# Performance work log

Measured on AMD Instinct MI355X. Metric: run time of the kernel, lower is better.

Reference implementation:

```python
import jax, jax.numpy as jnp
import numpy as np
import math

D = 2048            # fc_feat_size (hardcoded sqrt(2048) scale in source)
IMAGES = 20         # images_per_person
NEIGHBOR = 5        # neighbor_size (sliding window width)
T = IMAGES - NEIGHBOR + 1   # number of windows = 16
SCALE = 1.0 / math.sqrt(2048.0)


def _attention(x, Wq, bq, Wk, bk, Wv, bv):
    # x: [N, L, D] -> [N, L, D]; bmm-softmax-bmm as in source
    q = x @ Wq.T + bq
    k = x @ Wk.T + bk
    v = x @ Wv.T + bv
    dot = jnp.einsum('nld,nmd->nlm', q, k) * SCALE
    w = jax.nn.softmax(dot, axis=-1)
    return jnp.einsum('nlm,nmd->nld', w, v)


def _lstm_final(x, Wih, Whh, bih, bhh):
    # PyTorch-convention LSTM (gates i,f,g,o); x: [N, L, D] -> final hidden [N, H]
    N = x.shape[0]
    H = Whh.shape[1]
    xg = x @ Wih.T + (bih + bhh)   # [N, L, 4H] precompute input projections

    def step(carry, xt):
        h, c = carry
        gates = xt + h @ Whh.T
        i, f, g, o = jnp.split(gates, 4, axis=-1)
        c = jax.nn.sigmoid(f) * c + jax.nn.sigmoid(i) * jnp.tanh(g)
        h = jax.nn.sigmoid(o) * jnp.tanh(c)
        return (h, c), None

    init = (jnp.zeros((N, H), x.dtype), jnp.zeros((N, H), x.dtype))
    (h, _), _ = jax.lax.scan(step, init, jnp.swapaxes(xg, 0, 1))
    return h


def _layernorm(x, g, b, eps=1e-5):
    mu = jnp.mean(x, axis=-1, keepdims=True)
    var = jnp.var(x, axis=-1, keepdims=True)
    return (x - mu) * jax.lax.rsqrt(var + eps) * g + b


def setup_inputs() -> dict:
    key = jax.random.key(0)
    ks = iter(jax.random.split(key, 32))
    s = 0.02
    p = {}
    p['fc_feats'] = jax.random.normal(next(ks), (64, IMAGES, D), jnp.float32)
    for pre in ('nsa', 'sa'):
        for nm in ('Wq', 'Wk', 'Wv'):
            p[f'{pre}_{nm}'] = jax.random.normal(next(ks), (D, D), jnp.float32) * s
        for nm in ('bq', 'bk', 'bv'):
            p[f'{pre}_{nm}'] = jnp.zeros((D,), jnp.float32)
        p[f'{pre}_Wih'] = jax.random.normal(next(ks), (4 * D, D), jnp.float32) * s
        p[f'{pre}_Whh'] = jax.random.normal(next(ks), (4 * D, D), jnp.float32) * s
        p[f'{pre}_bih'] = jnp.zeros((4 * D,), jnp.float32)
        p[f'{pre}_bhh'] = jnp.zeros((4 * D,), jnp.float32)
    p['ln_g'] = jnp.ones((D,), jnp.float32)
    p['ln_b'] = jnp.zeros((D,), jnp.float32)
    return p


def reference(fc_feats,
              nsa_Wq, nsa_Wk, nsa_Wv, nsa_bq, nsa_bk, nsa_bv,
              nsa_Wih, nsa_Whh, nsa_bih, nsa_bhh,
              sa_Wq, sa_Wk, sa_Wv, sa_bq, sa_bk, sa_bv,
              sa_Wih, sa_Whh, sa_bih, sa_bhh,
              ln_g, ln_b):
    B = fc_feats.shape[0]
    # Sliding windows: window t covers images [t, t+NEIGHBOR) -> [B, T, W, D]
    idx = jnp.arange(T)[:, None] + jnp.arange(NEIGHBOR)[None, :]
    windows = fc_feats[:, idx]                       # [B, T, W, D]
    wflat = windows.reshape(B * T, NEIGHBOR, D)
    # NeighboringSelfAttention: attention within window + LSTM final state
    att = _attention(wflat, nsa_Wq, nsa_bq, nsa_Wk, nsa_bk, nsa_Wv, nsa_bv)
    nsa = _lstm_final(att, nsa_Wih, nsa_Whh, nsa_bih, nsa_bhh)  # [B*T, D]
    nsa_feats = nsa.reshape(B, T, D)
    new_nsa_feats = _layernorm(nsa_feats, ln_g, ln_b)
    # SelfAttention over the T window summaries + LSTM final state
    att2 = _attention(new_nsa_feats, sa_Wq, sa_bq, sa_Wk, sa_bk, sa_Wv, sa_bv)
    sa_feats = _lstm_final(att2, sa_Wih, sa_Whh, sa_bih, sa_bhh)  # [B, D]
    return (sa_feats, new_nsa_feats)
```

## Files before the change

kernel.cpp:

```cpp
#include <hip/hip_runtime.h>
#include <hip/hip_bf16.h>

typedef unsigned int  u32;
typedef unsigned short u16;

typedef __bf16 bf16x8 __attribute__((ext_vector_type(8)));
typedef float  f32x4  __attribute__((ext_vector_type(4)));

#define D2048 2048
#define SCALE 0.022097086912079612f

__device__ __forceinline__ u32 f2bfbits(float f) {
    u32 u = __float_as_uint(f);
    return (u + 0x7FFFu + ((u >> 16) & 1u)) >> 16;
}
__device__ __forceinline__ u32 pack2(float a, float b) {
    return f2bfbits(a) | (f2bfbits(b) << 16);
}
__device__ __forceinline__ float bf2f(u32 h) {
    return __uint_as_float(h << 16);
}
__device__ __forceinline__ void unpack8(uint4 v, float* f) {
    f[0] = bf2f(v.x & 0xFFFFu); f[1] = bf2f(v.x >> 16);
    f[2] = bf2f(v.y & 0xFFFFu); f[3] = bf2f(v.y >> 16);
    f[4] = bf2f(v.z & 0xFFFFu); f[5] = bf2f(v.z >> 16);
    f[6] = bf2f(v.w & 0xFFFFu); f[7] = bf2f(v.w >> 16);
}
__device__ __forceinline__ float sigmf(float x) { return 1.f / (1.f + __expf(-x)); }
__device__ __forceinline__ float tanhf_(float x) {
    x = fminf(15.f, fmaxf(-15.f, x));
    float e = __expf(2.f * x);
    return (e - 1.f) / (e + 1.f);
}

__device__ __forceinline__ void gload_lds16(const u16* g, u16* l) {
    __builtin_amdgcn_global_load_lds(
        (const __attribute__((address_space(1))) unsigned int*)g,
        (__attribute__((address_space(3))) unsigned int*)l,
        16, 0, 0);
}

struct CvtArgs {
    const float* src[8];
    u16*         dst[8];
    int          n4[8];
    int          nseg;
};
__global__ __launch_bounds__(256) void cvt_multi(CvtArgs a) {
    int stride = gridDim.x * 256;
    for (int s = 0; s < a.nseg; ++s) {
        const float4* S = reinterpret_cast<const float4*>(a.src[s]);
        uint2*        D = reinterpret_cast<uint2*>(a.dst[s]);
        int n4 = a.n4[s];
        for (int i = blockIdx.x * 256 + threadIdx.x; i < n4; i += stride) {
            float4 v = S[i];
            uint2 p;
            p.x = pack2(v.x, v.y);
            p.y = pack2(v.z, v.w);
            D[i] = p;
        }
    }
}

template <bool OUT_BF16>
__global__ __launch_bounds__(512, 2) void gemm256(const u16* __restrict__ A, int lda,
                                                  const u16* __restrict__ B,
                                                  void* __restrict__ C0,
                                                  int M, int N, int K) {
    __shared__ u16 Ab[2][16384];
    __shared__ u16 Bb[2][16384];

    const int tid  = threadIdx.x;
    const int lane = tid & 63;
    const int wid  = tid >> 6;
    const int wm   = wid >> 2;
    const int wn   = wid & 3;
    const int l15  = lane & 15, l4 = lane >> 4;
    const int rowBase = blockIdx.y * 256;
    const int colBase = blockIdx.x * 256;

    const int srow8 = lane >> 3;
    const int scw   = ((lane & 7) ^ srow8) * 8;
    const u16* gA = A + (size_t)(rowBase + wid * 8 + srow8) * lda + scw;
    const u16* gB = B + (size_t)(colBase + wid * 8 + srow8) * (size_t)K + scw;
    const int ldsW = wid * 512;

#define STAGE_A(buf, koff, q) \
    gload_lds16(gA + (size_t)((q) * 64) * lda + (koff), &Ab[buf][(q) * 4096 + ldsW])
#define STAGE_B(buf, koff, q) \
    gload_lds16(gB + (size_t)((q) * 64) * (size_t)K + (koff), &Bb[buf][(q) * 4096 + ldsW])

    f32x4 acc[8][4];
#pragma unroll
    for (int m = 0; m < 8; m++)
#pragma unroll
        for (int n = 0; n < 4; n++) acc[m][n] = f32x4{0.f, 0.f, 0.f, 0.f};

    const int nt = K >> 6;

#pragma unroll
    for (int q = 0; q < 4; ++q) { STAGE_A(0, 0, q); STAGE_B(0, 0, q); }

    const int swzA = (l15 & 7);

    for (int t = 0; t < nt; ++t) {
        const int cur = t & 1;
        const int nxt = cur ^ 1;
        const int kN  = (t + 1) << 6;
        const bool more = (t + 1 < nt);

        if (more) {
            STAGE_A(nxt, kN, 0);
            STAGE_A(nxt, kN, 1);
            asm volatile("s_waitcnt vmcnt(2)" ::: "memory");
        } else {
            asm volatile("s_waitcnt vmcnt(0)" ::: "memory");
        }
        __builtin_amdgcn_s_barrier();

        bf16x8 bfrag[4][2];
#pragma unroll
        for (int n = 0; n < 4; ++n)
#pragma unroll
            for (int kk = 0; kk < 2; ++kk)
                bfrag[n][kk] = *reinterpret_cast<const bf16x8*>(
                    &Bb[cur][(wn * 64 + n * 16 + l15) * 64 +
                             (((kk * 4 + l4) ^ swzA) * 8)]);

#pragma unroll
        for (int p = 0; p < 4; ++p) {
            bf16x8 afr[2][2];
#pragma unroll
            for (int mi = 0; mi < 2; ++mi)
#pragma unroll
                for (int kk = 0; kk < 2; ++kk)
                    afr[mi][kk] = *reinterpret_cast<const bf16x8*>(
                        &Ab[cur][(wm * 128 + (p * 2 + mi) * 16 + l15) * 64 +
                                 (((kk * 4 + l4) ^ swzA) * 8)]);
            if (more) {
                if (p == 0)      { STAGE_A(nxt, kN, 2); STAGE_A(nxt, kN, 3); }
                else if (p == 1) { STAGE_B(nxt, kN, 0); STAGE_B(nxt, kN, 1); }
                else if (p == 2) { STAGE_B(nxt, kN, 2); STAGE_B(nxt, kN, 3); }
            }
            __builtin_amdgcn_s_barrier();
            __builtin_amdgcn_sched_barrier(0);
            __builtin_amdgcn_s_setprio(1);
#pragma unroll
            for (int kk = 0; kk < 2; ++kk)
#pragma unroll
                for (int mi = 0; mi < 2; ++mi)
#pragma unroll
                    for (int n = 0; n < 4; ++n)
                        acc[p * 2 + mi][n] = __builtin_amdgcn_mfma_f32_16x16x32_bf16(
                            afr[mi][kk], bfrag[n][kk], acc[p * 2 + mi][n], 0, 0, 0);
            __builtin_amdgcn_s_setprio(0);
            __builtin_amdgcn_sched_barrier(0);
            __builtin_amdgcn_s_barrier();
        }
    }
#undef STAGE_A
#undef STAGE_B

#pragma unroll
    for (int m = 0; m < 8; ++m) {
        int row0 = rowBase + wm * 128 + m * 16 + l4 * 4;
#pragma unroll
        for (int n = 0; n < 4; ++n) {
            int col = colBase + wn * 64 + n * 16 + l15;
#pragma unroll
            for (int rr = 0; rr < 4; ++rr) {
                if (OUT_BF16)
                    ((u16*)C0)[(size_t)(row0 + rr) * N + col] = (u16)f2bfbits(acc[m][n][rr]);
                else
                    ((float*)C0)[(size_t)(row0 + rr) * N + col] = acc[m][n][rr];
            }
        }
    }
}

__global__ __launch_bounds__(256) void gemm_qkv(const u16* __restrict__ A,
                                                const u16* __restrict__ B0,
                                                const u16* __restrict__ B1,
                                                const u16* __restrict__ B2,
                                                const float* __restrict__ bias0,
                                                const float* __restrict__ bias1,
                                                const float* __restrict__ bias2,
                                                u16* __restrict__ Cout,
                                                size_t zCstride,
                                                int M, int N, int K) {
    __shared__ u16 Abuf[2][128 * 64];
    __shared__ u16 Bbuf[2][128 * 64];

    const int tid  = threadIdx.x;
    const int lane = tid & 63;
    const int wave = tid >> 6;
    const int wr   = (wave >> 1) * 64;
    const int wc   = (wave & 1) * 64;
    const int rowBase = blockIdx.y * 128;
    const int colBase = blockIdx.x * 128;
    const int l15 = lane & 15, l4 = lane >> 4;
    const int srow = lane >> 3;
    const int scol = (lane & 7) * 8;

    const int z = blockIdx.z;
    const u16* B      = (z == 0) ? B0 : ((z == 1) ? B1 : B2);
    const float* bias = (z == 0) ? bias0 : ((z == 1) ? bias1 : bias2);
    u16* C = Cout + (size_t)z * zCstride;

    const u16* ga = A + (size_t)(rowBase + wave * 32 + srow) * K + scol;
    const u16* gb = B + (size_t)(colBase + wave * 32 + srow) * K + scol;
    const int ldsOff = (wave * 32) * 64;

    f32x4 acc[4][4];
#pragma unroll
    for (int i = 0; i < 4; i++)
#pragma unroll
        for (int j = 0; j < 4; j++) acc[i][j] = f32x4{0.f, 0.f, 0.f, 0.f};

    const int nt = K >> 6;

#pragma unroll
    for (int i = 0; i < 4; ++i) {
        gload_lds16(ga + (size_t)(i * 8) * K, &Abuf[0][ldsOff + i * 8 * 64]);
        gload_lds16(gb + (size_t)(i * 8) * K, &Bbuf[0][ldsOff + i * 8 * 64]);
    }

    for (int t = 0; t < nt; ++t) {
        const int cur = t & 1;
        if (t + 1 < nt) {
            const int k1 = (t + 1) << 6;
#pragma unroll
            for (int i = 0; i < 4; ++i) {
                gload_lds16(ga + (size_t)(i * 8) * K + k1,
                            &Abuf[cur ^ 1][ldsOff + i * 8 * 64]);
                gload_lds16(gb + (size_t)(i * 8) * K + k1,
                            &Bbuf[cur ^ 1][ldsOff + i * 8 * 64]);
            }
            asm volatile("s_waitcnt vmcnt(8)" ::: "memory");
        } else {
            asm volatile("s_waitcnt vmcnt(0)" ::: "memory");
        }
        __builtin_amdgcn_s_barrier();
        __builtin_amdgcn_sched_barrier(0);
#pragma unroll
        for (int kk = 0; kk < 2; ++kk) {
            bf16x8 af[4], bfr[4];
#pragma unroll
            for (int i = 0; i < 4; i++) {
                af[i]  = *reinterpret_cast<const bf16x8*>(
                    &Abuf[cur][(wr + i * 16 + l15) * 64 + kk * 32 + l4 * 8]);
                bfr[i] = *reinterpret_cast<const bf16x8*>(
                    &Bbuf[cur][(wc + i * 16 + l15) * 64 + kk * 32 + l4 * 8]);
            }
#pragma unroll
            for (int i = 0; i < 4; i++)
#pragma unroll
                for (int j = 0; j < 4; j++)
                    acc[i][j] = __builtin_amdgcn_mfma_f32_16x16x32_bf16(af[i], bfr[j],
                                                                        acc[i][j], 0, 0, 0);
        }
        __builtin_amdgcn_sched_barrier(0);
        __builtin_amdgcn_s_barrier();
    }

#pragma unroll
    for (int i = 0; i < 4; i++) {
        int row0 = rowBase + wr + i * 16 + l4 * 4;
#pragma unroll
        for (int j = 0; j < 4; j++) {
            int col = colBase + wc + j * 16 + l15;
            float bv = bias[col];
#pragma unroll
            for (int rr = 0; rr < 4; rr++)
                C[(size_t)(row0 + rr) * N + col] = (u16)f2bfbits(acc[i][j][rr] + bv);
        }
    }
}

template <bool LAST>
__global__ __launch_bounds__(256) void gemm_gate128(
    const u16* __restrict__ A,
    const u16* __restrict__ B,
    const u16* __restrict__ xg,
    int xg_stride,
    const float* __restrict__ bih,
    const float* __restrict__ bhh,
    float* __restrict__ c,
    u16* __restrict__ hbf_out,
    float* __restrict__ hf,
    int K) {
    __shared__ u16 smem[32768];
    u16* Ab = smem;
    u16* Bb = smem + 16384;

    const int tid = threadIdx.x, lane = tid & 63, wave = tid >> 6;
    const int wr = (wave >> 1) * 64, wc = (wave & 1) * 64;
    const int l15 = lane & 15, l4 = lane >> 4;
    const int srow = lane >> 3, scol = (lane & 7) * 8;
    const int jBase = blockIdx.x * 32;
    const int rowBase = blockIdx.y * 128;

    const u16* ga = A + (size_t)(rowBase + wave * 32 + srow) * K + scol;
    const u16* gb[4];
#pragma unroll
    for (int i = 0; i < 4; ++i) {
        int lc = wave * 32 + i * 8 + srow;
        int br = jBase + (lc & 31) + (lc >> 5) * 2048;
        gb[i] = B + (size_t)br * K + scol;
    }
    const int ldsOff = (wave * 32) * 64;

    f32x4 acc[4][4];
#pragma unroll
    for (int i = 0; i < 4; i++)
#pragma unroll
        for (int j = 0; j < 4; j++) acc[i][j] = f32x4{0.f, 0.f, 0.f, 0.f};

    const int nt = K >> 6;
#pragma unroll
    for (int i = 0; i < 4; ++i) {
        gload_lds16(ga + (size_t)(i * 8) * K, &Ab[ldsOff + i * 8 * 64]);
        gload_lds16(gb[i], &Bb[ldsOff + i * 8 * 64]);
    }

    for (int t = 0; t < nt; ++t) {
        const int cur = (t & 1) * 8192;
        if (t + 1 < nt) {
            const int k1 = (t + 1) << 6;
            const int nxt = ((t + 1) & 1) * 8192;
#pragma unroll
            for (int i = 0; i < 4; ++i) {
                gload_lds16(ga + (size_t)(i * 8) * K + k1, &Ab[nxt + ldsOff + i * 8 * 64]);
                gload_lds16(gb[i] + k1, &Bb[nxt + ldsOff + i * 8 * 64]);
            }
            asm volatile("s_waitcnt vmcnt(8)" ::: "memory");
        } else {
            asm volatile("s_waitcnt vmcnt(0)" ::: "memory");
        }
        __builtin_amdgcn_s_barrier();
        __builtin_amdgcn_sched_barrier(0);
#pragma unroll
        for (int kk = 0; kk < 2; ++kk) {
            bf16x8 af[4], bfr[4];
#pragma unroll
            for (int i = 0; i < 4; i++) {
                af[i]  = *reinterpret_cast<const bf16x8*>(
                    &Ab[cur + (wr + i * 16 + l15) * 64 + kk * 32 + l4 * 8]);
                bfr[i] = *reinterpret_cast<const bf16x8*>(
                    &Bb[cur + (wc + i * 16 + l15) * 64 + kk * 32 + l4 * 8]);
            }
#pragma unroll
            for (int i = 0; i < 4; i++)
#pragma unroll
                for (int j = 0; j < 4; j++)
                    acc[i][j] = __builtin_amdgcn_mfma_f32_16x16x32_bf16(af[i], bfr[j],
                                                                        acc[i][j], 0, 0, 0);
        }
        __builtin_amdgcn_sched_barrier(0);
        __builtin_amdgcn_s_barrier();
    }

    float* Cs = (float*)smem;
#pragma unroll
    for (int i = 0; i < 4; i++)
#pragma unroll
        for (int j = 0; j < 4; j++)
#pragma unroll
            for (int rr = 0; rr < 4; rr++)
                Cs[(wr + i * 16 + l4 * 4 + rr) * 128 + (wc + j * 16 + l15)] =
                    acc[i][j][rr];
    __syncthreads();

    const int j  = tid & 31;
    const int rb = tid >> 5;
    const int gj = jBase + j;
    const float bi_ = bih[gj]        + bhh[gj];
    const float bf_ = bih[gj + 2048] + bhh[gj + 2048];
    const float bg_ = bih[gj + 4096] + bhh[gj + 4096];
    const float bo_ = bih[gj + 6144] + bhh[gj + 6144];
#pragma unroll
    for (int k = 0; k < 16; ++k) {
        int r = rb * 16 + k;
        int n = rowBase + r;
        const u16* xr = xg + (size_t)n * xg_stride;
        float gi = Cs[r * 128 + j]      + bf2f((u32)xr[gj])        + bi_;
        float gf = Cs[r * 128 + 32 + j] + bf2f((u32)xr[gj + 2048]) + bf_;
        float gg = Cs[r * 128 + 64 + j] + bf2f((u32)xr[gj + 4096]) + bg_;
        float go = Cs[r * 128 + 96 + j] + bf2f((u32)xr[gj + 6144]) + bo_;
        size_t idx = (size_t)n * 2048 + gj;
        float cc = c[idx];
        float cn = sigmf(gf) * cc + sigmf(gi) * tanhf_(gg);
        float hn = sigmf(go) * tanhf_(cn);
        c[idx] = cn;
        hbf_out[idx] = (u16)f2bfbits(hn);
        if (LAST) hf[idx] = hn;
    }
}

__global__ __launch_bounds__(256) void gemm_gate64(
    const u16* __restrict__ A,
    const u16* __restrict__ B,
    const u16* __restrict__ xg,
    int xg_stride,
    const float* __restrict__ bih,
    const float* __restrict__ bhh,
    float* __restrict__ c,
    u16* __restrict__ hbf_out,
    float* __restrict__ hf,
    int K) {
    __shared__ u16 smem[24576];
    u16* Ab = smem;
    u16* Bb = smem + 8192;

    const int tid = threadIdx.x, lane = tid & 63, wave = tid >> 6;
    const int l15 = lane & 15, l4 = lane >> 4;
    const int srow = lane >> 3, scol = (lane & 7) * 8;
    const int jBase = blockIdx.x * 32;

    const u16* ga = A + (size_t)(wave * 16 + srow) * K + scol;
    const u16* gb[4];
#pragma unroll
    for (int i = 0; i < 4; ++i) {
        int lc = wave * 32 + i * 8 + srow;
        int br = jBase + (lc & 31) + (lc >> 5) * 2048;
        gb[i] = B + (size_t)br * K + scol;
    }
    const int laOff = (wave * 16) * 64;
    const int lbOff = (wave * 32) * 64;

    f32x4 acc[4][2];
#pragma unroll
    for (int i = 0; i < 4; i++)
#pragma unroll
        for (int j = 0; j < 2; j++) acc[i][j] = f32x4{0.f, 0.f, 0.f, 0.f};

    const int nt = K >> 6;
#pragma unroll
    for (int i = 0; i < 2; ++i)
        gload_lds16(ga + (size_t)(i * 8) * K, &Ab[laOff + i * 8 * 64]);
#pragma unroll
    for (int i = 0; i < 4; ++i)
        gload_lds16(gb[i], &Bb[lbOff + i * 8 * 64]);

    for (int t = 0; t < nt; ++t) {
        const int curA = (t & 1) * 4096;
        const int curB = (t & 1) * 8192;
        if (t + 1 < nt) {
            const int k1 = (t + 1) << 6;
            const int nxA = ((t + 1) & 1) * 4096;
            const int nxB = ((t + 1) & 1) * 8192;
#pragma unroll
            for (int i = 0; i < 2; ++i)
                gload_lds16(ga + (size_t)(i * 8) * K + k1, &Ab[nxA + laOff + i * 8 * 64]);
#pragma unroll
            for (int i = 0; i < 4; ++i)
                gload_lds16(gb[i] + k1, &Bb[nxB + lbOff + i * 8 * 64]);
            asm volatile("s_waitcnt vmcnt(6)" ::: "memory");
        } else {
            asm volatile("s_waitcnt vmcnt(0)" ::: "memory");
        }
        __builtin_amdgcn_s_barrier();
        __builtin_amdgcn_sched_barrier(0);
#pragma unroll
        for (int kk = 0; kk < 2; ++kk) {
            bf16x8 af[4], bfr[2];
#pragma unroll
            for (int i = 0; i < 4; i++)
                af[i] = *reinterpret_cast<const bf16x8*>(
                    &Ab[curA + (i * 16 + l15) * 64 + kk * 32 + l4 * 8]);
#pragma unroll
            for (int j = 0; j < 2; j++)
                bfr[j] = *reinterpret_cast<const bf16x8*>(
                    &Bb[curB + (wave * 32 + j * 16 + l15) * 64 + kk * 32 + l4 * 8]);
#pragma unroll
            for (int i = 0; i < 4; i++)
#pragma unroll
                for (int j = 0; j < 2; j++)
                    acc[i][j] = __builtin_amdgcn_mfma_f32_16x16x32_bf16(af[i], bfr[j],
                                                                        acc[i][j], 0, 0, 0);
        }
        __builtin_amdgcn_sched_barrier(0);
        __builtin_amdgcn_s_barrier();
    }

    float* Cs = (float*)smem;
#pragma unroll
    for (int i = 0; i < 4; i++)
#pragma unroll
        for (int j = 0; j < 2; j++)
#pragma unroll
            for (int rr = 0; rr < 4; rr++)
                Cs[(i * 16 + l4 * 4 + rr) * 128 + (wave * 32 + j * 16 + l15)] =
                    acc[i][j][rr];
    __syncthreads();

    const int j  = tid & 31;
    const int rb = tid >> 5;
    const int gj = jBase + j;
    const float bi_ = bih[gj]        + bhh[gj];
    const float bf_ = bih[gj + 2048] + bhh[gj + 2048];
    const float bg_ = bih[gj + 4096] + bhh[gj + 4096];
    const float bo_ = bih[gj + 6144] + bhh[gj + 6144];
#pragma unroll
    for (int k = 0; k < 8; ++k) {
        int n = rb * 8 + k;
        const u16* xr = xg + (size_t)n * xg_stride;
        float gi = Cs[n * 128 + j]      + bf2f((u32)xr[gj])        + bi_;
        float gf = Cs[n * 128 + 32 + j] + bf2f((u32)xr[gj + 2048]) + bf_;
        float gg = Cs[n * 128 + 64 + j] + bf2f((u32)xr[gj + 4096]) + bg_;
        float go = Cs[n * 128 + 96 + j] + bf2f((u32)xr[gj + 6144]) + bo_;
        size_t idx = (size_t)n * 2048 + gj;
        float cc = c[idx];
        float cn = sigmf(gf) * cc + sigmf(gi) * tanhf_(gg);
        float hn = sigmf(go) * tanhf_(cn);
        c[idx] = cn;
        hbf_out[idx] = (u16)f2bfbits(hn);
        if (hf) hf[idx] = hn;
    }
}

__global__ __launch_bounds__(256) void lstm_gate0(const u16* __restrict__ xg,
                                                  int xg_stride,
                                                  const float* __restrict__ bih,
                                                  const float* __restrict__ bhh,
                                                  float* __restrict__ c,
                                                  u16* __restrict__ hbf,
                                                  int rows) {
    int idx = blockIdx.x * 256 + threadIdx.x;
    int total = rows * 512;
    if (idx >= total) return;
    int n  = idx >> 9;
    int j4 = (idx & 511) * 4;

    const u16* xr = xg + (size_t)n * xg_stride + j4;
    float4 gi, gf, gg, go;
    {
        uint2 ri = *reinterpret_cast<const uint2*>(xr);
        uint2 rg = *reinterpret_cast<const uint2*>(xr + 4096);
        uint2 ro = *reinterpret_cast<const uint2*>(xr + 6144);
        gi = {bf2f(ri.x & 0xFFFFu), bf2f(ri.x >> 16), bf2f(ri.y & 0xFFFFu), bf2f(ri.y >> 16)};
        gg = {bf2f(rg.x & 0xFFFFu), bf2f(rg.x >> 16), bf2f(rg.y & 0xFFFFu), bf2f(rg.y >> 16)};
        go = {bf2f(ro.x & 0xFFFFu), bf2f(ro.x >> 16), bf2f(ro.y & 0xFFFFu), bf2f(ro.y >> 16)};
    }
    float4 bi1 = *reinterpret_cast<const float4*>(bih + j4);
    float4 bg1 = *reinterpret_cast<const float4*>(bih + 4096 + j4);
    float4 bo1 = *reinterpret_cast<const float4*>(bih + 6144 + j4);
    float4 bi2 = *reinterpret_cast<const float4*>(bhh + j4);
    float4 bg2 = *reinterpret_cast<const float4*>(bhh + 4096 + j4);
    float4 bo2 = *reinterpret_cast<const float4*>(bhh + 6144 + j4);

    gi.x += bi1.x + bi2.x; gi.y += bi1.y + bi2.y; gi.z += bi1.z + bi2.z; gi.w += bi1.w + bi2.w;
    gg.x += bg1.x + bg2.x; gg.y += bg1.y + bg2.y; gg.z += bg1.z + bg2.z; gg.w += bg1.w + bg2.w;
    go.x += bo1.x + bo2.x; go.y += bo1.y + bo2.y; go.z += bo1.z + bo2.z; go.w += bo1.w + bo2.w;

    float cx = sigmf(gi.x) * tanhf_(gg.x);
    float cy = sigmf(gi.y) * tanhf_(gg.y);
    float cz = sigmf(gi.z) * tanhf_(gg.z);
    float cw = sigmf(gi.w) * tanhf_(gg.w);
    float hx = sigmf(go.x) * tanhf_(cx);
    float hy = sigmf(go.y) * tanhf_(cy);
    float hz = sigmf(go.z) * tanhf_(cz);
    float hw_ = sigmf(go.w) * tanhf_(cw);

    float4 co = {cx, cy, cz, cw};
    *reinterpret_cast<float4*>(c + (size_t)n * 2048 + j4) = co;
    uint2 hp;
    hp.x = pack2(hx, hy);
    hp.y = pack2(hz, hw_);
    *reinterpret_cast<uint2*>(hbf + (size_t)n * 2048 + j4) = hp;
}

__global__ __launch_bounds__(256) void attn_win5(const u16* __restrict__ q0,
                                                 const u16* __restrict__ k0,
                                                 const u16* __restrict__ v0,
                                                 u16* __restrict__ att) {
    int n = blockIdx.x;
    int b = n >> 4, t = n & 15;
    int tid = threadIdx.x, lane = tid & 63, wave = tid >> 6;
    int d0 = tid * 8;
    size_t base = (size_t)(b * 20 + t) * D2048;

    float qv[5][8];
#pragma unroll
    for (int i = 0; i < 5; i++) {
        uint4 v = *reinterpret_cast<const uint4*>(q0 + base + (size_t)i * D2048 + d0);
        unpack8(v, qv[i]);
    }
    float part[25];
#pragma unroll
    for (int p = 0; p < 25; p++) part[p] = 0.f;
#pragma unroll
    for (int m = 0; m < 5; m++) {
        float kv[8];
        uint4 v = *reinterpret_cast<const uint4*>(k0 + base + (size_t)m * D2048 + d0);
        unpack8(v, kv);
#pragma unroll
        for (int l = 0; l < 5; l++)
#pragma unroll
            for (int j = 0; j < 8; j++) part[l * 5 + m] += qv[l][j] * kv[j];
    }
#pragma unroll
    for (int p = 0; p < 25; p++) {
        float s = part[p];
#pragma unroll
        for (int msk = 32; msk; msk >>= 1) s += __shfl_xor(s, msk, 64);
        part[p] = s;
    }
    __shared__ float wred[4][25];
    __shared__ float wmat[25];
    if (lane == 0) {
#pragma unroll
        for (int p = 0; p < 25; p++) wred[wave][p] = part[p];
    }
    __syncthreads();
    if (tid < 5) {
        int l = tid;
        float dv[5], mx = -1e30f;
#pragma unroll
        for (int m = 0; m < 5; m++) {
            dv[m] = (wred[0][l * 5 + m] + wred[1][l * 5 + m] + wred[2][l * 5 + m] +
                     wred[3][l * 5 + m]) * SCALE;
            mx = fmaxf(mx, dv[m]);
        }
        float ssum = 0.f;
#pragma unroll
        for (int m = 0; m < 5; m++) { dv[m] = __expf(dv[m] - mx); ssum += dv[m]; }
        float inv = 1.f / ssum;
#pragma unroll
        for (int m = 0; m < 5; m++) wmat[l * 5 + m] = dv[m] * inv;
    }
    __syncthreads();

    float oacc[5][8];
#pragma unroll
    for (int l = 0; l < 5; l++)
#pragma unroll
        for (int j = 0; j < 8; j++) oacc[l][j] = 0.f;
#pragma unroll
    for (int m = 0; m < 5; m++) {
        float vv[8];
        uint4 v = *reinterpret_cast<const uint4*>(v0 + base + (size_t)m * D2048 + d0);
        unpack8(v, vv);
#pragma unroll
        for (int l = 0; l < 5; l++) {
            float w = wmat[l * 5 + m];
#pragma unroll
            for (int j = 0; j < 8; j++) oacc[l][j] += w * vv[j];
        }
    }
#pragma unroll
    for (int l = 0; l < 5; l++) {
        uint4 p;
        p.x = pack2(oacc[l][0], oacc[l][1]);
        p.y = pack2(oacc[l][2], oacc[l][3]);
        p.z = pack2(oacc[l][4], oacc[l][5]);
        p.w = pack2(oacc[l][6], oacc[l][7]);
        *reinterpret_cast<uint4*>(att + (size_t)(n * 5 + l) * D2048 + d0) = p;
    }
}

__global__ __launch_bounds__(256) void attn_seq16(const u16* __restrict__ q2,
                                                  const u16* __restrict__ k2,
                                                  const u16* __restrict__ v2,
                                                  u16* __restrict__ att2) {
    int r = blockIdx.x;
    int b = r >> 4;
    int tid = threadIdx.x, lane = tid & 63, wave = tid >> 6;
    int d0 = tid * 8;
    size_t kbase = (size_t)b * 16 * D2048;

    float qv[8];
    {
        uint4 v = *reinterpret_cast<const uint4*>(q2 + (size_t)r * D2048 + d0);
        unpack8(v, qv);
    }
    float part[16];
#pragma unroll
    for (int m = 0; m < 16; m++) part[m] = 0.f;
#pragma unroll
    for (int m = 0; m < 16; m++) {
        float kv[8];
        uint4 v = *reinterpret_cast<const uint4*>(k2 + kbase + (size_t)m * D2048 + d0);
        unpack8(v, kv);
#pragma unroll
        for (int j = 0; j < 8; j++) part[m] += qv[j] * kv[j];
    }
#pragma unroll
    for (int m = 0; m < 16; m++) {
        float s = part[m];
#pragma unroll
        for (int msk = 32; msk; msk >>= 1) s += __shfl_xor(s, msk, 64);
        part[m] = s;
    }
    __shared__ float wred[4][16];
    __shared__ float wmat[16];
    if (lane == 0) {
#pragma unroll
        for (int m = 0; m < 16; m++) wred[wave][m] = part[m];
    }
    __syncthreads();
    if (tid == 0) {
        float dv[16], mx = -1e30f;
#pragma unroll
        for (int m = 0; m < 16; m++) {
            dv[m] = (wred[0][m] + wred[1][m] + wred[2][m] + wred[3][m]) * SCALE;
            mx = fmaxf(mx, dv[m]);
        }
        float ssum = 0.f;
#pragma unroll
        for (int m = 0; m < 16; m++) { dv[m] = __expf(dv[m] - mx); ssum += dv[m]; }
        float inv = 1.f / ssum;
#pragma unroll
        for (int m = 0; m < 16; m++) wmat[m] = dv[m] * inv;
    }
    __syncthreads();

    float oacc[8];
#pragma unroll
    for (int j = 0; j < 8; j++) oacc[j] = 0.f;
#pragma unroll
    for (int m = 0; m < 16; m++) {
        float vv[8];
        uint4 v = *reinterpret_cast<const uint4*>(v2 + kbase + (size_t)m * D2048 + d0);
        unpack8(v, vv);
        float w = wmat[m];
#pragma unroll
        for (int j = 0; j < 8; j++) oacc[j] += w * vv[j];
    }
    uint4 p;
    p.x = pack2(oacc[0], oacc[1]);
    p.y = pack2(oacc[2], oacc[3]);
    p.z = pack2(oacc[4], oacc[5]);
    p.w = pack2(oacc[6], oacc[7]);
    *reinterpret_cast<uint4*>(att2 + (size_t)r * D2048 + d0) = p;
}

__global__ __launch_bounds__(256) void layernorm_k(const float* __restrict__ x,
                                                   const float* __restrict__ g,
                                                   const float* __restrict__ b,
                                                   float* __restrict__ y,
                                                   u16* __restrict__ ybf) {
    int row = blockIdx.x;
    int tid = threadIdx.x, lane = tid & 63, wave = tid >> 6;
    const float* xr = x + (size_t)row * D2048;
    int j = tid * 8;
    float4 v1 = *reinterpret_cast<const float4*>(xr + j);
    float4 v2 = *reinterpret_cast<const float4*>(xr + j + 4);
    float s  = v1.x + v1.y + v1.z + v1.w + v2.x + v2.y + v2.z + v2.w;
    float s2 = v1.x * v1.x + v1.y * v1.y + v1.z * v1.z + v1.w * v1.w +
               v2.x * v2.x + v2.y * v2.y + v2.z * v2.z + v2.w * v2.w;
#pragma unroll
    for (int msk = 32; msk; msk >>= 1) {
        s  += __shfl_xor(s, msk, 64);
        s2 += __shfl_xor(s2, msk, 64);
    }
    __shared__ float red[4][2];
    if (lane == 0) { red[wave][0] = s; red[wave][1] = s2; }
    __syncthreads();
    s  = red[0][0] + red[1][0] + red[2][0] + red[3][0];
    s2 = red[0][1] + red[1][1] + red[2][1] + red[3][1];
    float mu  = s * (1.f / 2048.f);
    float var = s2 * (1.f / 2048.f) - mu * mu;
    float rs  = __frsqrt_rn(var + 1e-5f);

    float4 g1 = *reinterpret_cast<const float4*>(g + j);
    float4 g2 = *reinterpret_cast<const float4*>(g + j + 4);
    float4 b1 = *reinterpret_cast<const float4*>(b + j);
    float4 b2 = *reinterpret_cast<const float4*>(b + j + 4);
    float o[8];
    o[0] = (v1.x - mu) * rs * g1.x + b1.x;
    o[1] = (v1.y - mu) * rs * g1.y + b1.y;
    o[2] = (v1.z - mu) * rs * g1.z + b1.z;
    o[3] = (v1.w - mu) * rs * g1.w + b1.w;
    o[4] = (v2.x - mu) * rs * g2.x + b2.x;
    o[5] = (v2.y - mu) * rs * g2.y + b2.y;
    o[6] = (v2.z - mu) * rs * g2.z + b2.z;
    o[7] = (v2.w - mu) * rs * g2.w + b2.w;
    float4 o1 = {o[0], o[1], o[2], o[3]};
    float4 o2 = {o[4], o[5], o[6], o[7]};
    float* yr = y + (size_t)row * D2048;
    *reinterpret_cast<float4*>(yr + j)     = o1;
    *reinterpret_cast<float4*>(yr + j + 4) = o2;
    uint4 p;
    p.x = pack2(o[0], o[1]);
    p.y = pack2(o[2], o[3]);
    p.z = pack2(o[4], o[5]);
    p.w = pack2(o[6], o[7]);
    *reinterpret_cast<uint4*>(ybf + (size_t)row * D2048 + j) = p;
}

static inline void launch_qkv(hipStream_t s, const u16* A, const u16* Wq,
                              const u16* Wk, const u16* Wv, const float* bq,
                              const float* bk, const float* bv, u16* out,
                              int M, int N, int K) {
    dim3 grid(N / 128, M / 128, 3);
    gemm_qkv<<<grid, 256, 0, s>>>(A, Wq, Wk, Wv, bq, bk, bv, out,
                                  (size_t)M * N, M, N, K);
}

extern "C" void kernel_launch(void* const* d_in, const int* in_sizes, int n_in,
                              void* d_out, int out_size, void* d_ws, size_t ws_size,
                              hipStream_t stream) {
    const float* fc      = (const float*)d_in[0];
    const float* nsa_Wq  = (const float*)d_in[1];
    const float* nsa_Wk  = (const float*)d_in[2];
    const float* nsa_Wv  = (const float*)d_in[3];
    const float* nsa_bq  = (const float*)d_in[4];
    const float* nsa_bk  = (const float*)d_in[5];
    const float* nsa_bv  = (const float*)d_in[6];
    const float* nsa_Wih = (const float*)d_in[7];
    const float* nsa_Whh = (const float*)d_in[8];
    const float* nsa_bih = (const float*)d_in[9];
    const float* nsa_bhh = (const float*)d_in[10];
    const float* sa_Wq   = (const float*)d_in[11];
    const float* sa_Wk   = (const float*)d_in[12];
    const float* sa_Wv   = (const float*)d_in[13];
    const float* sa_bq   = (const float*)d_in[14];
    const float* sa_bk   = (const float*)d_in[15];
    const float* sa_bv   = (const float*)d_in[16];
    const float* sa_Wih  = (const float*)d_in[17];
    const float* sa_Whh  = (const float*)d_in[18];
    const float* sa_bih  = (const float*)d_in[19];
    const float* sa_bhh  = (const float*)d_in[20];
    const float* ln_g    = (const float*)d_in[21];
    const float* ln_b    = (const float*)d_in[22];

    float* outF   = (float*)d_out;
    float* out_sa = outF;
    float* out_ln = outF + 131072;

    char* W = (char*)d_ws;
    u16* W_q   = (u16*)(W + 0);
    u16* W_k   = (u16*)(W + 8388608);
    u16* W_v   = (u16*)(W + 16777216);
    u16* W_ih  = (u16*)(W + 25165824);
    u16* W_hh1 = (u16*)(W + 58720256);
    u16* W_hh2 = (u16*)(W + 92274688);
    u16*   Xbf  = (u16*)(W + 125829120);
    u16*   q0   = (u16*)(W + 131072000);
    u16*   att1 = (u16*)(W + 146800640);
    u16*   xg   = (u16*)(W + 167772160);
    float* h1    = (float*)(W + 0);
    float* c1    = (float*)(W + 8388608);
    u16*   hbfA  = (u16*)(W + 16777216);
    u16*   hbfB  = (u16*)(W + 131072000);
    u16*   lnbf  = Xbf;
    u16*   q2    = q0;
    u16*   att2  = att1;
    float* c2    = (float*)(W + 148373504);
    u16*   h2bfA = (u16*)(W + 148897792);
    u16*   h2bfB = (u16*)(W + 149422080);

    {
        CvtArgs a{};
        a.src[0] = fc;      a.dst[0] = Xbf;   a.n4[0] = 655360;
        a.src[1] = nsa_Wq;  a.dst[1] = W_q;   a.n4[1] = 1048576;
        a.src[2] = nsa_Wk;  a.dst[2] = W_k;   a.n4[2] = 1048576;
        a.src[3] = nsa_Wv;  a.dst[3] = W_v;   a.n4[3] = 1048576;
        a.src[4] = nsa_Wih; a.dst[4] = W_ih;  a.n4[4] = 4194304;
        a.src[5] = nsa_Whh; a.dst[5] = W_hh1; a.n4[5] = 4194304;
        a.src[6] = sa_Whh;  a.dst[6] = W_hh2; a.n4[6] = 4194304;
        a.nseg = 7;
        cvt_multi<<<2048, 256, 0, stream>>>(a);
    }

    launch_qkv(stream, Xbf, W_q, W_k, W_v, nsa_bq, nsa_bk, nsa_bv, q0, 1280, 2048, 2048);

    attn_win5<<<1024, 256, 0, stream>>>(q0, q0 + 2621440, q0 + 5242880, att1);

    gemm256<true><<<dim3(32, 20), 512, 0, stream>>>(att1, 2048, W_ih, xg,
                                                    5120, 8192, 2048);

    lstm_gate0<<<2048, 256, 0, stream>>>(xg, 40960, nsa_bih, nsa_bhh, c1, hbfA, 1024);
    {
        u16* hin = hbfA;
        for (int t = 1; t < 5; ++t) {
            u16* hout = (t & 1) ? hbfB : hbfA;
            if (t == 4)
                gemm_gate128<true><<<dim3(64, 8), 256, 0, stream>>>(
                    hin, W_hh1, xg + (size_t)t * 8192, 40960, nsa_bih, nsa_bhh,
                    c1, hout, h1, 2048);
            else
                gemm_gate128<false><<<dim3(64, 8), 256, 0, stream>>>(
                    hin, W_hh1, xg + (size_t)t * 8192, 40960, nsa_bih, nsa_bhh,
                    c1, hout, nullptr, 2048);
            hin = hout;
        }
    }

    layernorm_k<<<1024, 256, 0, stream>>>(h1, ln_g, ln_b, out_ln, lnbf);

    {
        CvtArgs a{};
        a.src[0] = sa_Wq;  a.dst[0] = W_q;  a.n4[0] = 1048576;
        a.src[1] = sa_Wk;  a.dst[1] = W_k;  a.n4[1] = 1048576;
        a.src[2] = sa_Wv;  a.dst[2] = W_v;  a.n4[2] = 1048576;
        a.src[3] = sa_Wih; a.dst[3] = W_ih; a.n4[3] = 4194304;
        a.nseg = 4;
        cvt_multi<<<2048, 256, 0, stream>>>(a);
    }

    launch_qkv(stream, lnbf, W_q, W_k, W_v, sa_bq, sa_bk, sa_bv, q2, 1024, 2048, 2048);

    attn_seq16<<<1024, 256, 0, stream>>>(q2, q2 + 2097152, q2 + 4194304, att2);

    gemm256<true><<<dim3(32, 4), 512, 0, stream>>>(att2, 2048, W_ih, xg,
                                                   1024, 8192, 2048);

    lstm_gate0<<<128, 256, 0, stream>>>(xg, 131072, sa_bih, sa_bhh, c2, h2bfA, 64);
    {
        u16* hin = h2bfA;
        for (int t = 1; t < 16; ++t) {
            u16* hout = (t & 1) ? h2bfB : h2bfA;
            gemm_gate64<<<dim3(64), 256, 0, stream>>>(
                hin, W_hh2, xg + (size_t)t * 8192, 131072, sa_bih, sa_bhh,
                c2, hout, (t == 15) ? out_sa : nullptr, 2048);
            hin = hout;
        }
    }
}
```

Baseline: 1.171 ms.

## Split SA LSTM recurrent gate GEMM across more blocks and use 128-tile input GEMM

The second-stage LSTM recurrent step now launches 256 blocks, each owning 8 hidden units, instead of 64 blocks of 32. The goal is to spread the serial 15-step recurrence over more CUs, at the cost of lower per-block reuse of the h tile, which is now reloaded by every block. The SA input-projection GEMM also switches from a 256-thread-tile kernel on a 32x4 grid to a new 128x128-tile kernel on a 64x8 grid, for better CU occupancy. An unused float4 variable is removed.

```diff
diff --git a/kernel.cpp b/kernel.cpp
--- a/kernel.cpp
+++ b/kernel.cpp
@@ -277,6 +277,93 @@
     }
 }
 
+__global__ __launch_bounds__(256) void gemm128_bf(const u16* __restrict__ A,
+                                                  const u16* __restrict__ B,
+                                                  u16* __restrict__ C,
+                                                  int M, int N, int K) {
+    __shared__ u16 Abuf[2][128 * 64];
+    __shared__ u16 Bbuf[2][128 * 64];
+
+    const int tid  = threadIdx.x;
+    const int lane = tid & 63;
+    const int wave = tid >> 6;
+    const int wr   = (wave >> 1) * 64;
+    const int wc   = (wave & 1) * 64;
+    const int rowBase = blockIdx.y * 128;
+    const int colBase = blockIdx.x * 128;
+    const int l15 = lane & 15, l4 = lane >> 4;
+    const int srow = lane >> 3;
+    const int scol = (lane & 7) * 8;
+
+    const u16* ga = A + (size_t)(rowBase + wave * 32 + srow) * K + scol;
+    const u16* gb = B + (size_t)(colBase + wave * 32 + srow) * K + scol;
+    const int ldsOff = (wave * 32) * 64;
+
+    f32x4 acc[4][4];
+#pragma unroll
+    for (int i = 0; i < 4; i++)
+#pragma unroll
+        for (int j = 0; j < 4; j++) acc[i][j] = f32x4{0.f, 0.f, 0.f, 0.f};
+
+    const int nt = K >> 6;
+
+#pragma unroll
+    for (int i = 0; i < 4; ++i) {
+        gload_lds16(ga + (size_t)(i * 8) * K, &Abuf[0][ldsOff + i * 8 * 64]);
+        gload_lds16(gb + (size_t)(i * 8) * K, &Bbuf[0][ldsOff + i * 8 * 64]);
+    }
+
+    for (int t = 0; t < nt; ++t) {
+        const int cur = t & 1;
+        if (t + 1 < nt) {
+            const int k1 = (t + 1) << 6;
+#pragma unroll
+            for (int i = 0; i < 4; ++i) {
+                gload_lds16(ga + (size_t)(i * 8) * K + k1,
+                            &Abuf[cur ^ 1][ldsOff + i * 8 * 64]);
+                gload_lds16(gb + (size_t)(i * 8) * K + k1,
+                            &Bbuf[cur ^ 1][ldsOff + i * 8 * 64]);
+            }
+            asm volatile("s_waitcnt vmcnt(8)" ::: "memory");
+        } else {
+            asm volatile("s_waitcnt vmcnt(0)" ::: "memory");
+        }
+        __builtin_amdgcn_s_barrier();
+        __builtin_amdgcn_sched_barrier(0);
+#pragma unroll
+        for (int kk = 0; kk < 2; ++kk) {
+            bf16x8 af[4], bfr[4];
+#pragma unroll
+            for (int i = 0; i < 4; i++) {
+                af[i]  = *reinterpret_cast<const bf16x8*>(
+                    &Abuf[cur][(wr + i * 16 + l15) * 64 + kk * 32 + l4 * 8]);
+                bfr[i] = *reinterpret_cast<const bf16x8*>(
+                    &Bbuf[cur][(wc + i * 16 + l15) * 64 + kk * 32 + l4 * 8]);
+            }
+#pragma unroll
+            for (int i = 0; i < 4; i++)
+#pragma unroll
+                for (int j = 0; j < 4; j++)
+                    acc[i][j] = __builtin_amdgcn_mfma_f32_16x16x32_bf16(af[i], bfr[j],
+                                                                        acc[i][j], 0, 0, 0);
+        }
+        __builtin_amdgcn_sched_barrier(0);
+        __builtin_amdgcn_s_barrier();
+    }
+
+#pragma unroll
+    for (int i = 0; i < 4; i++) {
+        int row0 = rowBase + wr + i * 16 + l4 * 4;
+#pragma unroll
+        for (int j = 0; j < 4; j++) {
+            int col = colBase + wc + j * 16 + l15;
+#pragma unroll
+            for (int rr = 0; rr < 4; rr++)
+                C[(size_t)(row0 + rr) * N + col] = (u16)f2bfbits(acc[i][j][rr]);
+        }
+    }
+}
+
 template <bool LAST>
 __global__ __launch_bounds__(256) void gemm_gate128(
     const u16* __restrict__ A,
@@ -397,7 +484,7 @@
     }
 }
 
-__global__ __launch_bounds__(256) void gemm_gate64(
+__global__ __launch_bounds__(256) void gemm_gate64v2(
     const u16* __restrict__ A,
     const u16* __restrict__ B,
     const u16* __restrict__ xg,
@@ -408,54 +495,39 @@
     u16* __restrict__ hbf_out,
     float* __restrict__ hf,
     int K) {
-    __shared__ u16 smem[24576];
+    __shared__ u16 smem[12288];
     u16* Ab = smem;
     u16* Bb = smem + 8192;
 
     const int tid = threadIdx.x, lane = tid & 63, wave = tid >> 6;
     const int l15 = lane & 15, l4 = lane >> 4;
     const int srow = lane >> 3, scol = (lane & 7) * 8;
-    const int jBase = blockIdx.x * 32;
+    const int jb = blockIdx.x;
 
     const u16* ga = A + (size_t)(wave * 16 + srow) * K + scol;
-    const u16* gb[4];
-#pragma unroll
-    for (int i = 0; i < 4; ++i) {
-        int lc = wave * 32 + i * 8 + srow;
-        int br = jBase + (lc & 31) + (lc >> 5) * 2048;
-        gb[i] = B + (size_t)br * K + scol;
-    }
-    const int laOff = (wave * 16) * 64;
-    const int lbOff = (wave * 32) * 64;
-
-    f32x4 acc[4][2];
-#pragma unroll
-    for (int i = 0; i < 4; i++)
-#pragma unroll
-        for (int j = 0; j < 2; j++) acc[i][j] = f32x4{0.f, 0.f, 0.f, 0.f};
+    const u16* gb = B + (size_t)(jb * 8 + srow + wave * 2048) * K + scol;
+    const int aOff = (wave * 16) * 64;
+    const int bOff = (wave * 8) * 64;
+
+    f32x4 acc0 = f32x4{0.f, 0.f, 0.f, 0.f};
+    f32x4 acc1 = f32x4{0.f, 0.f, 0.f, 0.f};
 
     const int nt = K >> 6;
-#pragma unroll
-    for (int i = 0; i < 2; ++i)
-        gload_lds16(ga + (size_t)(i * 8) * K, &Ab[laOff + i * 8 * 64]);
-#pragma unroll
-    for (int i = 0; i < 4; ++i)
-        gload_lds16(gb[i], &Bb[lbOff + i * 8 * 64]);
+    gload_lds16(ga,                 &Ab[aOff]);
+    gload_lds16(ga + (size_t)8 * K, &Ab[aOff + 512]);
+    gload_lds16(gb,                 &Bb[bOff]);
 
     for (int t = 0; t < nt; ++t) {
         const int curA = (t & 1) * 4096;
-        const int curB = (t & 1) * 8192;
+        const int curB = (t & 1) * 2048;
         if (t + 1 < nt) {
             const int k1 = (t + 1) << 6;
             const int nxA = ((t + 1) & 1) * 4096;
-            const int nxB = ((t + 1) & 1) * 8192;
-#pragma unroll
-            for (int i = 0; i < 2; ++i)
-                gload_lds16(ga + (size_t)(i * 8) * K + k1, &Ab[nxA + laOff + i * 8 * 64]);
-#pragma unroll
-            for (int i = 0; i < 4; ++i)
-                gload_lds16(gb[i] + k1, &Bb[nxB + lbOff + i * 8 * 64]);
-            asm volatile("s_waitcnt vmcnt(6)" ::: "memory");
+            const int nxB = ((t + 1) & 1) * 2048;
+            gload_lds16(ga + k1,                 &Ab[nxA + aOff]);
+            gload_lds16(ga + (size_t)8 * K + k1, &Ab[nxA + aOff + 512]);
+            gload_lds16(gb + k1,                 &Bb[nxB + bOff]);
+            asm volatile("s_waitcnt vmcnt(3)" ::: "memory");
         } else {
             asm volatile("s_waitcnt vmcnt(0)" ::: "memory");
         }
@@ -463,53 +535,45 @@
         __builtin_amdgcn_sched_barrier(0);
 #pragma unroll
         for (int kk = 0; kk < 2; ++kk) {
-            bf16x8 af[4], bfr[2];
-#pragma unroll
-            for (int i = 0; i < 4; i++)
-                af[i] = *reinterpret_cast<const bf16x8*>(
-                    &Ab[curA + (i * 16 + l15) * 64 + kk * 32 + l4 * 8]);
-#pragma unroll
-            for (int j = 0; j < 2; j++)
-                bfr[j] = *reinterpret_cast<const bf16x8*>(
-                    &Bb[curB + (wave * 32 + j * 16 + l15) * 64 + kk * 32 + l4 * 8]);
-#pragma unroll
-            for (int i = 0; i < 4; i++)
-#pragma unroll
-                for (int j = 0; j < 2; j++)
-                    acc[i][j] = __builtin_amdgcn_mfma_f32_16x16x32_bf16(af[i], bfr[j],
-                                                                        acc[i][j], 0, 0, 0);
+            bf16x8 af = *reinterpret_cast<const bf16x8*>(
+                &Ab[curA + (wave * 16 + l15) * 64 + kk * 32 + l4 * 8]);
+            bf16x8 b0 = *reinterpret_cast<const bf16x8*>(
+                &Bb[curB + (l15) * 64 + kk * 32 + l4 * 8]);
+            bf16x8 b1 = *reinterpret_cast<const bf16x8*>(
+                &Bb[curB + (16 + l15) * 64 + kk * 32 + l4 * 8]);
+            acc0 = __builtin_amdgcn_mfma_f32_16x16x32_bf16(af, b0, acc0, 0, 0, 0);
+            acc1 = __builtin_amdgcn_mfma_f32_16x16x32_bf16(af, b1, acc1, 0, 0, 0);
         }
         __builtin_amdgcn_sched_barrier(0);
         __builtin_amdgcn_s_barrier();
     }
 
     float* Cs = (float*)smem;
-#pragma unroll
-    for (int i = 0; i < 4; i++)
-#pragma unroll
-        for (int j = 0; j < 2; j++)
-#pragma unroll
-            for (int rr = 0; rr < 4; rr++)
-                Cs[(i * 16 + l4 * 4 + rr) * 128 + (wave * 32 + j * 16 + l15)] =
-                    acc[i][j][rr];
+    {
+        int row0 = wave * 16 + l4 * 4;
+#pragma unroll
+        for (int rr = 0; rr < 4; ++rr) {
+            Cs[(row0 + rr) * 32 + l15]      = acc0[rr];
+            Cs[(row0 + rr) * 32 + 16 + l15] = acc1[rr];
+        }
+    }
     __syncthreads();
 
-    const int j  = tid & 31;
-    const int rb = tid >> 5;
-    const int gj = jBase + j;
+    const int j  = tid & 7;
+    const int gj = jb * 8 + j;
     const float bi_ = bih[gj]        + bhh[gj];
     const float bf_ = bih[gj + 2048] + bhh[gj + 2048];
     const float bg_ = bih[gj + 4096] + bhh[gj + 4096];
     const float bo_ = bih[gj + 6144] + bhh[gj + 6144];
 #pragma unroll
-    for (int k = 0; k < 8; ++k) {
-        int n = rb * 8 + k;
-        const u16* xr = xg + (size_t)n * xg_stride;
-        float gi = Cs[n * 128 + j]      + bf2f((u32)xr[gj])        + bi_;
-        float gf = Cs[n * 128 + 32 + j] + bf2f((u32)xr[gj + 2048]) + bf_;
-        float gg = Cs[n * 128 + 64 + j] + bf2f((u32)xr[gj + 4096]) + bg_;
-        float go = Cs[n * 128 + 96 + j] + bf2f((u32)xr[gj + 6144]) + bo_;
-        size_t idx = (size_t)n * 2048 + gj;
+    for (int k = 0; k < 2; ++k) {
+        int row = (tid >> 3) + k * 32;
+        const u16* xr = xg + (size_t)row * xg_stride;
+        float gi = Cs[row * 32 + j]      + bf2f((u32)xr[gj])        + bi_;
+        float gf = Cs[row * 32 + 8 + j]  + bf2f((u32)xr[gj + 2048]) + bf_;
+        float gg = Cs[row * 32 + 16 + j] + bf2f((u32)xr[gj + 4096]) + bg_;
+        float go = Cs[row * 32 + 24 + j] + bf2f((u32)xr[gj + 6144]) + bo_;
+        size_t idx = (size_t)row * 2048 + gj;
         float cc = c[idx];
         float cn = sigmf(gf) * cc + sigmf(gi) * tanhf_(gg);
         float hn = sigmf(go) * tanhf_(cn);
@@ -533,7 +597,7 @@
     int j4 = (idx & 511) * 4;
 
     const u16* xr = xg + (size_t)n * xg_stride + j4;
-    float4 gi, gf, gg, go;
+    float4 gi, gg, go;
     {
         uint2 ri = *reinterpret_cast<const uint2*>(xr);
         uint2 rg = *reinterpret_cast<const uint2*>(xr + 4096);
@@ -904,15 +968,14 @@
 
     attn_seq16<<<1024, 256, 0, stream>>>(q2, q2 + 2097152, q2 + 4194304, att2);
 
-    gemm256<true><<<dim3(32, 4), 512, 0, stream>>>(att2, 2048, W_ih, xg,
-                                                   1024, 8192, 2048);
+    gemm128_bf<<<dim3(64, 8), 256, 0, stream>>>(att2, W_ih, xg, 1024, 8192, 2048);
 
     lstm_gate0<<<128, 256, 0, stream>>>(xg, 131072, sa_bih, sa_bhh, c2, h2bfA, 64);
     {
         u16* hin = h2bfA;
         for (int t = 1; t < 16; ++t) {
             u16* hout = (t & 1) ? h2bfB : h2bfA;
-            gemm_gate64<<<dim3(64), 256, 0, stream>>>(
+            gemm_gate64v2<<<dim3(256), 256, 0, stream>>>(
                 hin, W_hh2, xg + (size_t)t * 8192, 131072, sa_bih, sa_bhh,
                 c2, hout, (t == 15) ? out_sa : nullptr, 2048);
             hin = hout;
```

After: 953.7 us, median of 3. -18.6%, faster.
